# Optimization experiments

Hardware: AMD Instinct MI355X
Metric: run time of the kernel (lower is better)

Reference implementation:

```python
import jax, jax.numpy as jnp
import numpy as np

SIZE = 4096  # core_size(16) ** nr_cores(3)


def setup_inputs() -> dict:
    key = jax.random.key(0)
    k_x, k0, k1, k2, kb = jax.random.split(key, 5)
    d, r = 16, 64
    # std per TT.init_core: sigma = (t * sqrt(r)**(1-c))**(1/c), t=1/sqrt(size), c=3
    t = 1.0 / np.sqrt(SIZE)
    sigma = float((t * np.sqrt(r) ** (1 - 3)) ** (1.0 / 3))
    x = jax.random.normal(k_x, (4, 2048, SIZE), dtype=jnp.float32)
    g0 = sigma * jax.random.normal(k0, (1, d, d, r), dtype=jnp.float32)
    g1 = sigma * jax.random.normal(k1, (r, d, d, r), dtype=jnp.float32)
    g2 = sigma * jax.random.normal(k2, (r, d, d, 1), dtype=jnp.float32)
    bias = np.sqrt(1.0 / SIZE) * jax.random.uniform(kb, (SIZE,), dtype=jnp.float32, minval=-1.0, maxval=1.0)
    return {"x": x, "g0": g0, "g1": g1, "g2": g2, "bias": bias}


def reference(x, g0, g1, g2, bias):
    # to_matrix: chain of einsum contractions over TT cores
    G = g0[0]  # (d, d, r)
    G = jnp.einsum('ija,aklb->ijklb', G, g1)      # (d,d,d,d,r)
    G = jnp.einsum('ijkla,amnb->ijklmnb', G, g2)  # (d,d,d,d,d,d,1)
    G = G.reshape(SIZE, SIZE)
    # forward: flatten leading dims, dense matmul + bias, restore shape
    X = x.reshape(-1, SIZE)
    out = X @ G + bias
    return out.reshape(*x.shape[:-1], SIZE)
```

## Files before the change

kernel.cpp:

```cpp
#include <hip/hip_runtime.h>
#include <stdint.h>

#define DI __device__ __forceinline__

using floatx4 = __attribute__((ext_vector_type(4))) float;
using short8  = __attribute__((ext_vector_type(8))) short;

DI uint16_t f2b(float f) {
  uint32_t u = __float_as_uint(f);
  return (uint16_t)((u + 0x7FFFu + ((u >> 16) & 1u)) >> 16);
}

DI void async_cp16(const uint16_t* g, uint16_t* l) {
  __builtin_amdgcn_global_load_lds(
      (const __attribute__((address_space(1))) void*)g,
      (__attribute__((address_space(3))) void*)l, 16, 0, 0);
}

__global__ __launch_bounds__(256)
void cvt_bf16(const float* __restrict__ x, uint16_t* __restrict__ y) {
  long i = ((long)blockIdx.x * 256 + threadIdx.x) * 8;
  float4 a = *(const float4*)(x + i);
  float4 b = *(const float4*)(x + i + 4);
  union { uint16_t u[8]; uint4 v; } o;
  o.u[0] = f2b(a.x); o.u[1] = f2b(a.y); o.u[2] = f2b(a.z); o.u[3] = f2b(a.w);
  o.u[4] = f2b(b.x); o.u[5] = f2b(b.y); o.u[6] = f2b(b.z); o.u[7] = f2b(b.w);
  *(uint4*)(y + i) = o.v;
}

__global__ __launch_bounds__(256)
void tt_t1(const float* __restrict__ g0, const float* __restrict__ g1,
           uint16_t* __restrict__ t1) {
  __shared__ float g0s[64 * 64];
  __shared__ float g1s[64 * 128];
  const int rowbase = blockIdx.x * 64;
  const int colbase = blockIdx.y * 128;
  const int t = threadIdx.x;

  for (int f = t; f < 4096; f += 256) g0s[f] = g0[rowbase * 64 + f];
  for (int f = t; f < 8192; f += 256) {
    int a = f >> 7, c = f & 127;
    g1s[f] = g1[(long)a * 16384 + colbase + c];
  }
  __syncthreads();

  const int tx = t & 31;
  const int ty = t >> 5;
  const int c0 = tx * 4;
  const int r0 = ty * 8;

  float acc[8][4];
  #pragma unroll
  for (int r = 0; r < 8; ++r)
    #pragma unroll
    for (int c = 0; c < 4; ++c) acc[r][c] = 0.f;

  for (int a4 = 0; a4 < 16; ++a4) {
    float g0r[8][4];
    #pragma unroll
    for (int r = 0; r < 8; ++r)
      *(float4*)&g0r[r][0] = *(const float4*)&g0s[(r0 + r) * 64 + a4 * 4];
    #pragma unroll
    for (int e = 0; e < 4; ++e) {
      float4 bv4 = *(const float4*)&g1s[(a4 * 4 + e) * 128 + c0];
      float bv[4] = {bv4.x, bv4.y, bv4.z, bv4.w};
      #pragma unroll
      for (int r = 0; r < 8; ++r)
        #pragma unroll
        for (int c = 0; c < 4; ++c)
          acc[r][c] += g0r[r][e] * bv[c];
    }
  }

  #pragma unroll
  for (int r = 0; r < 8; ++r) {
    ushort4 o;
    o.x = f2b(acc[r][0]); o.y = f2b(acc[r][1]);
    o.z = f2b(acc[r][2]); o.w = f2b(acc[r][3]);
    *(ushort4*)&t1[(long)(rowbase + r0 + r) * 16384 + colbase + c0] = o;
  }
}

__global__ __launch_bounds__(256)
void g2t_build(const float* __restrict__ g2, uint16_t* __restrict__ g2t) {
  int f = blockIdx.x * 256 + threadIdx.x;
  int mn = f >> 6, b = f & 63;
  g2t[f] = f2b(g2[b * 256 + mn]);
}

__global__ __launch_bounds__(256)
void transpose_t1(const uint16_t* __restrict__ src, uint16_t* __restrict__ dst) {
  __shared__ uint16_t tile[64][68];
  const int cb = blockIdx.x * 64;
  const int rb = blockIdx.y * 64;
  const int t = threadIdx.x;
  {
    const int c4 = (t & 15) * 4;
    const int r  = t >> 4;
    #pragma unroll
    for (int p = 0; p < 4; ++p) {
      int rr = r + p * 16;
      *(ushort4*)&tile[rr][c4] = *(const ushort4*)&src[(long)(rb + rr) * 1024 + cb + c4];
    }
  }
  __syncthreads();
  {
    const int r4 = (t & 15) * 4;
    const int c  = t >> 4;
    #pragma unroll
    for (int p = 0; p < 4; ++p) {
      int cc = c + p * 16;
      ushort4 o;
      o.x = tile[r4 + 0][cc]; o.y = tile[r4 + 1][cc];
      o.z = tile[r4 + 2][cc]; o.w = tile[r4 + 3][cc];
      *(ushort4*)&dst[(long)(cb + cc) * 4096 + rb + r4] = o;
    }
  }
}

template <bool OUT_BF16, bool ADD_BIAS>
__global__ __launch_bounds__(256)
void gemm_bt(const uint16_t* __restrict__ A, int ldA, int zA,
             const uint16_t* __restrict__ Bt, int ldB,
             void* __restrict__ Cv, int ldC, int colOff,
             const float* __restrict__ bias, int K) {
  __shared__ __align__(16) uint16_t As[128 * 32];
  __shared__ __align__(16) uint16_t Bs[128 * 32];

  const int bm = blockIdx.x * 128;
  const int bn = blockIdx.y * 128;
  const int z  = blockIdx.z;
  const int tid  = threadIdx.x;
  const int wave = tid >> 6;
  const int lane = tid & 63;
  const int wm = (wave >> 1) * 64;
  const int wn = (wave & 1) * 64;

  const uint16_t* Ab = A + (long)bm * ldA + (long)zA * z;
  const uint16_t* Bb = Bt + (long)bn * ldB;

  const int srow = lane >> 2;
  const int scol = (lane & 3) * 8;

  floatx4 acc[4][4];
  #pragma unroll
  for (int i = 0; i < 4; ++i)
    #pragma unroll
    for (int j = 0; j < 4; ++j)
      acc[i][j] = (floatx4){0.f, 0.f, 0.f, 0.f};

  const int fr = lane & 15;
  const int fk = (lane >> 4) * 8;

  for (int k0 = 0; k0 < K; k0 += 32) {
    __syncthreads();
    #pragma unroll
    for (int t = 0; t < 2; ++t) {
      const int rblk = wave * 2 + t;
      async_cp16(Ab + (long)(rblk * 16 + srow) * ldA + k0 + scol, &As[rblk * 16 * 32]);
      async_cp16(Bb + (long)(rblk * 16 + srow) * ldB + k0 + scol, &Bs[rblk * 16 * 32]);
    }
    __syncthreads();

    short8 af[4], bg[4];
    #pragma unroll
    for (int i = 0; i < 4; ++i)
      af[i] = *(const short8*)&As[(wm + i * 16 + fr) * 32 + fk];
    #pragma unroll
    for (int j = 0; j < 4; ++j)
      bg[j] = *(const short8*)&Bs[(wn + j * 16 + fr) * 32 + fk];

    #pragma unroll
    for (int i = 0; i < 4; ++i)
      #pragma unroll
      for (int j = 0; j < 4; ++j)
        acc[i][j] = __builtin_amdgcn_mfma_f32_16x16x32_bf16(af[i], bg[j], acc[i][j], 0, 0, 0);
  }

  const int colq = lane & 15;
  const int rowq = (lane >> 4) * 4;
  const long coff = (long)colOff * z;
  #pragma unroll
  for (int j = 0; j < 4; ++j) {
    const int col = bn + wn + j * 16 + colq;
    float bv = 0.f;
    if constexpr (ADD_BIAS) bv = bias[coff + col];
    #pragma unroll
    for (int i = 0; i < 4; ++i)
      #pragma unroll
      for (int r = 0; r < 4; ++r) {
        const int row = bm + wm + i * 16 + rowq + r;
        float v = acc[i][j][r] + bv;
        if constexpr (OUT_BF16)
          ((uint16_t*)Cv)[(long)row * ldC + coff + col] = f2b(v);
        else
          ((float*)Cv)[(long)row * ldC + coff + col] = v;
      }
  }
}

static constexpr long XBF_OFF = 0;
static constexpr long T1_OFF  = 67108864;
static constexpr long T1T_OFF = 75497472;
static constexpr long V_OFF   = 83886080;
static constexpr long G2T_OFF = 100663296;

extern "C" void kernel_launch(void* const* d_in, const int* in_sizes, int n_in,
                              void* d_out, int out_size, void* d_ws, size_t ws_size,
                              hipStream_t stream) {
  const float* x    = (const float*)d_in[0];
  const float* g0   = (const float*)d_in[1];
  const float* g1   = (const float*)d_in[2];
  const float* g2   = (const float*)d_in[3];
  const float* bias = (const float*)d_in[4];
  float* out = (float*)d_out;

  char* ws = (char*)d_ws;
  uint16_t* Xbf = (uint16_t*)(ws + XBF_OFF);
  uint16_t* T1  = (uint16_t*)(ws + T1_OFF);
  uint16_t* T1t = (uint16_t*)(ws + T1T_OFF);
  uint16_t* V   = (uint16_t*)(ws + V_OFF);
  uint16_t* G2T = (uint16_t*)(ws + G2T_OFF);

  cvt_bf16<<<16384, 256, 0, stream>>>(x, Xbf);
  tt_t1<<<dim3(4, 128), 256, 0, stream>>>(g0, g1, T1);
  g2t_build<<<64, 256, 0, stream>>>(g2, G2T);
  transpose_t1<<<dim3(16, 64), 256, 0, stream>>>(T1, T1t);
  gemm_bt<true, false><<<dim3(64, 8, 1), 256, 0, stream>>>(
      Xbf, 4096, 0, T1t, 4096, (void*)V, 1024, 0, nullptr, 4096);
  gemm_bt<false, true><<<dim3(64, 2, 16), 256, 0, stream>>>(
      V, 1024, 64, G2T, 64, (void*)out, 4096, 256, bias, 64);
}
```

Before: 385.9 us.

## Fuse second TT-core GEMM into first GEMM epilogue via LDS-staged intermediate

The first GEMM now keeps its 128x128 tile of the intermediate V in shared memory as bf16 and immediately multiplies it by the transposed g2 core inside the same block, writing the fp32 output plus bias directly. This removes the global round-trip of V and a separate launch. The g2 transpose/convert is also folded into the T1 transpose kernel, saving one more launch. In exchange the fused kernel uses more LDS and registers (launch bounds 2), which may lower occupancy for the main K loop.

Result: faster. 350.8 us (-9.1%).

```diff
diff --git a/kernel.cpp b/kernel.cpp
--- a/kernel.cpp
+++ b/kernel.cpp
@@ -82,18 +82,21 @@
 }
 
 __global__ __launch_bounds__(256)
-void g2t_build(const float* __restrict__ g2, uint16_t* __restrict__ g2t) {
-  int f = blockIdx.x * 256 + threadIdx.x;
-  int mn = f >> 6, b = f & 63;
-  g2t[f] = f2b(g2[b * 256 + mn]);
-}
-
-__global__ __launch_bounds__(256)
-void transpose_t1(const uint16_t* __restrict__ src, uint16_t* __restrict__ dst) {
+void transpose_t1(const uint16_t* __restrict__ src, uint16_t* __restrict__ dst,
+                  const float* __restrict__ g2, uint16_t* __restrict__ g2t) {
   __shared__ uint16_t tile[64][68];
   const int cb = blockIdx.x * 64;
   const int rb = blockIdx.y * 64;
   const int t = threadIdx.x;
+
+  if (blockIdx.y == 0) {
+    #pragma unroll
+    for (int p = 0; p < 4; ++p) {
+      int f = blockIdx.x * 1024 + p * 256 + t;
+      int mn = f >> 6, b = f & 63;
+      g2t[f] = f2b(g2[b * 256 + mn]);
+    }
+  }
   {
     const int c4 = (t & 15) * 4;
     const int r  = t >> 4;
@@ -118,26 +121,27 @@
   }
 }
 
-template <bool OUT_BF16, bool ADD_BIAS>
-__global__ __launch_bounds__(256)
-void gemm_bt(const uint16_t* __restrict__ A, int ldA, int zA,
-             const uint16_t* __restrict__ Bt, int ldB,
-             void* __restrict__ Cv, int ldC, int colOff,
-             const float* __restrict__ bias, int K) {
+#define VSTRIDE 136
+__global__ __launch_bounds__(256, 2)
+void gemm_fused(const uint16_t* __restrict__ A,
+                const uint16_t* __restrict__ Bt,
+                const uint16_t* __restrict__ g2t,
+                const float* __restrict__ bias,
+                float* __restrict__ out) {
   __shared__ __align__(16) uint16_t As[128 * 32];
   __shared__ __align__(16) uint16_t Bs[128 * 32];
+  __shared__ __align__(16) uint16_t Vs[128 * VSTRIDE];
 
   const int bm = blockIdx.x * 128;
   const int bn = blockIdx.y * 128;
-  const int z  = blockIdx.z;
   const int tid  = threadIdx.x;
   const int wave = tid >> 6;
   const int lane = tid & 63;
   const int wm = (wave >> 1) * 64;
   const int wn = (wave & 1) * 64;
 
-  const uint16_t* Ab = A + (long)bm * ldA + (long)zA * z;
-  const uint16_t* Bb = Bt + (long)bn * ldB;
+  const uint16_t* Ab = A + (long)bm * 4096;
+  const uint16_t* Bb = Bt + (long)bn * 4096;
 
   const int srow = lane >> 2;
   const int scol = (lane & 3) * 8;
@@ -152,13 +156,13 @@
   const int fr = lane & 15;
   const int fk = (lane >> 4) * 8;
 
-  for (int k0 = 0; k0 < K; k0 += 32) {
+  for (int k0 = 0; k0 < 4096; k0 += 32) {
     __syncthreads();
     #pragma unroll
     for (int t = 0; t < 2; ++t) {
       const int rblk = wave * 2 + t;
-      async_cp16(Ab + (long)(rblk * 16 + srow) * ldA + k0 + scol, &As[rblk * 16 * 32]);
-      async_cp16(Bb + (long)(rblk * 16 + srow) * ldB + k0 + scol, &Bs[rblk * 16 * 32]);
+      async_cp16(Ab + (long)(rblk * 16 + srow) * 4096 + k0 + scol, &As[rblk * 16 * 32]);
+      async_cp16(Bb + (long)(rblk * 16 + srow) * 4096 + k0 + scol, &Bs[rblk * 16 * 32]);
     }
     __syncthreads();
 
@@ -179,31 +183,72 @@
 
   const int colq = lane & 15;
   const int rowq = (lane >> 4) * 4;
-  const long coff = (long)colOff * z;
-  #pragma unroll
-  for (int j = 0; j < 4; ++j) {
-    const int col = bn + wn + j * 16 + colq;
-    float bv = 0.f;
-    if constexpr (ADD_BIAS) bv = bias[coff + col];
-    #pragma unroll
-    for (int i = 0; i < 4; ++i)
-      #pragma unroll
-      for (int r = 0; r < 4; ++r) {
-        const int row = bm + wm + i * 16 + rowq + r;
-        float v = acc[i][j][r] + bv;
-        if constexpr (OUT_BF16)
-          ((uint16_t*)Cv)[(long)row * ldC + coff + col] = f2b(v);
-        else
-          ((float*)Cv)[(long)row * ldC + coff + col] = v;
-      }
+  __syncthreads();
+  #pragma unroll
+  for (int i = 0; i < 4; ++i)
+    #pragma unroll
+    for (int j = 0; j < 4; ++j)
+      #pragma unroll
+      for (int r = 0; r < 4; ++r)
+        Vs[(wm + i * 16 + rowq + r) * VSTRIDE + wn + j * 16 + colq] = f2b(acc[i][j][r]);
+  __syncthreads();
+
+  const int bsel   = (wave >> 1) * 64;
+  const int mnBase = (wave & 1) * 128;
+  const long ocol0 = (long)blockIdx.y * 512 + (wave >> 1) * 256 + mnBase;
+
+  short8 bg2[8][2];
+  #pragma unroll
+  for (int jn = 0; jn < 8; ++jn)
+    #pragma unroll
+    for (int ks = 0; ks < 2; ++ks)
+      bg2[jn][ks] = *(const short8*)&g2t[(mnBase + jn * 16 + fr) * 64 + ks * 32 + fk];
+
+  float bvs[8];
+  #pragma unroll
+  for (int jn = 0; jn < 8; ++jn)
+    bvs[jn] = bias[ocol0 + jn * 16 + colq];
+
+  #pragma unroll
+  for (int pass = 0; pass < 4; ++pass) {
+    floatx4 acc2[2][8];
+    #pragma unroll
+    for (int im = 0; im < 2; ++im)
+      #pragma unroll
+      for (int jn = 0; jn < 8; ++jn)
+        acc2[im][jn] = (floatx4){0.f, 0.f, 0.f, 0.f};
+
+    short8 af2[2][2];
+    #pragma unroll
+    for (int im = 0; im < 2; ++im)
+      #pragma unroll
+      for (int ks = 0; ks < 2; ++ks)
+        af2[im][ks] = *(const short8*)&Vs[(pass * 32 + im * 16 + fr) * VSTRIDE + bsel + ks * 32 + fk];
+
+    #pragma unroll
+    for (int im = 0; im < 2; ++im)
+      #pragma unroll
+      for (int jn = 0; jn < 8; ++jn)
+        #pragma unroll
+        for (int ks = 0; ks < 2; ++ks)
+          acc2[im][jn] = __builtin_amdgcn_mfma_f32_16x16x32_bf16(af2[im][ks], bg2[jn][ks], acc2[im][jn], 0, 0, 0);
+
+    #pragma unroll
+    for (int jn = 0; jn < 8; ++jn)
+      #pragma unroll
+      for (int im = 0; im < 2; ++im)
+        #pragma unroll
+        for (int r = 0; r < 4; ++r) {
+          const int row = bm + pass * 32 + im * 16 + rowq + r;
+          out[(long)row * 4096 + ocol0 + jn * 16 + colq] = acc2[im][jn][r] + bvs[jn];
+        }
   }
 }
 
 static constexpr long XBF_OFF = 0;
 static constexpr long T1_OFF  = 67108864;
 static constexpr long T1T_OFF = 75497472;
-static constexpr long V_OFF   = 83886080;
-static constexpr long G2T_OFF = 100663296;
+static constexpr long G2T_OFF = 83886080;
 
 extern "C" void kernel_launch(void* const* d_in, const int* in_sizes, int n_in,
                               void* d_out, int out_size, void* d_ws, size_t ws_size,
@@ -219,15 +264,10 @@
   uint16_t* Xbf = (uint16_t*)(ws + XBF_OFF);
   uint16_t* T1  = (uint16_t*)(ws + T1_OFF);
   uint16_t* T1t = (uint16_t*)(ws + T1T_OFF);
-  uint16_t* V   = (uint16_t*)(ws + V_OFF);
   uint16_t* G2T = (uint16_t*)(ws + G2T_OFF);
 
   cvt_bf16<<<16384, 256, 0, stream>>>(x, Xbf);
   tt_t1<<<dim3(4, 128), 256, 0, stream>>>(g0, g1, T1);
-  g2t_build<<<64, 256, 0, stream>>>(g2, G2T);
-  transpose_t1<<<dim3(16, 64), 256, 0, stream>>>(T1, T1t);
-  gemm_bt<true, false><<<dim3(64, 8, 1), 256, 0, stream>>>(
-      Xbf, 4096, 0, T1t, 4096, (void*)V, 1024, 0, nullptr, 4096);
-  gemm_bt<false, true><<<dim3(64, 2, 16), 256, 0, stream>>>(
-      V, 1024, 64, G2T, 64, (void*)out, 4096, 256, bias, 64);
-}
+  transpose_t1<<<dim3(16, 64), 256, 0, stream>>>(T1, T1t, g2, G2T);
+  gemm_fused<<<dim3(64, 8), 256, 0, stream>>>(Xbf, T1t, G2T, bias, out);
+}
```
